# Kernel optimization log

Hardware: AMD Instinct MI355X
Metric: run time of the kernel (lower is better)

The kernel has to match this reference:

```python
import jax, jax.numpy as jnp
import numpy as np

B, S, IN, OUT = 4, 2048, 4096, 4096


def setup_inputs() -> dict:
    key = jax.random.key(0)
    k_x, k_q, k_s, k_z, k_b = jax.random.split(key, 5)
    x = jax.random.normal(k_x, (B, S, IN), dtype=jnp.float32)
    # packed int4 weights: each int holds two unsigned nibbles (inputs 2r and 2r+1)
    qweight = jax.random.randint(k_q, (IN // 2, OUT), 0, 256, dtype=jnp.int32)
    # per-output-channel scales (positive) and zeros (zeros = zero_point * scale in pack())
    scales = jax.random.uniform(k_s, (OUT, 1), minval=0.01, maxval=0.05, dtype=jnp.float32)
    zeros = jax.random.normal(k_z, (OUT, 1), dtype=jnp.float32) * 0.1
    bias = jax.random.normal(k_b, (OUT,), dtype=jnp.float32) * 0.02
    return {"x": x, "qweight": qweight, "scales": scales, "zeros": zeros, "bias": bias}


def _dequant_weight(qweight, scales, zeros):
    # unpack two 4-bit values per packed element along the input dim
    low = qweight & 0xF            # input index 2r
    high = (qweight >> 4) & 0xF    # input index 2r+1
    w_int = jnp.stack([low, high], axis=1).reshape(-1, qweight.shape[1])  # (IN, OUT)
    zp = jnp.round(zeros / scales)  # integer zero point per output channel, (OUT,1)
    # w = (q - zp) * scale, broadcast per output column
    return (w_int.astype(jnp.float32) - zp.T) * scales.T  # (IN, OUT)


def reference(x, qweight, scales, zeros, bias):
    w = _dequant_weight(qweight, scales, zeros)          # (IN, OUT) fp32
    y = jnp.einsum('bsi,io->bso', x.astype(jnp.float32), w) + bias
    return y.astype(x.dtype)
```

## Files before the change

### kernel.cpp

```cpp
#include <hip/hip_runtime.h>
#include <hip/hip_bf16.h>
#include <stdint.h>

#define M_TOT 8192
#define N_TOT 4096
#define K_TOT 4096
#define BM 128
#define BN 128
#define BKI 128
#define NTI (K_TOT / BKI)

typedef short s16x8 __attribute__((ext_vector_type(8)));
typedef float f32x4 __attribute__((ext_vector_type(4)));
typedef int   i32x4 __attribute__((ext_vector_type(4)));
typedef char  i8x16 __attribute__((ext_vector_type(16)));

__device__ __forceinline__ short f2bf(float f) {
    unsigned int u = __float_as_uint(f);
    u = (u + 0x7fffu + ((u >> 16) & 1u)) >> 16;
    return (short)u;
}

__device__ __forceinline__ void async_copy16(const void* g, void* l) {
    __builtin_amdgcn_global_load_lds(
        (const __attribute__((address_space(1))) void*)g,
        (__attribute__((address_space(3))) void*)l, 16, 0, 0);
}

__global__ __launch_bounds__(256)
void prep(const float* __restrict__ x, const int* __restrict__ qw,
          char* __restrict__ xq, char* __restrict__ wq,
          float* __restrict__ sxv, float* __restrict__ sumv) {
    __shared__ float rmax[4], rsum[4];
    __shared__ char tile[256 * 64];
    const int t = threadIdx.x;

    if (blockIdx.x < M_TOT) {
        const int row = blockIdx.x;
        const float* xp = x + (size_t)row * K_TOT + t * 16;
        f32x4 f[4];
        float amax = 0.f, sum = 0.f;
        #pragma unroll
        for (int i = 0; i < 4; ++i) {
            f[i] = *(const f32x4*)(xp + i * 4);
            #pragma unroll
            for (int j = 0; j < 4; ++j) {
                amax = fmaxf(amax, fabsf(f[i][j]));
                sum += f[i][j];
            }
        }
        #pragma unroll
        for (int s = 1; s < 64; s <<= 1) {
            amax = fmaxf(amax, __shfl_xor(amax, s, 64));
            sum += __shfl_xor(sum, s, 64);
        }
        const int wv = t >> 6;
        if ((t & 63) == 0) { rmax[wv] = amax; rsum[wv] = sum; }
        __syncthreads();
        amax = fmaxf(fmaxf(rmax[0], rmax[1]), fmaxf(rmax[2], rmax[3]));
        sum  = rsum[0] + rsum[1] + rsum[2] + rsum[3];
        const float inv = amax > 0.f ? 127.0f / amax : 0.f;
        i8x16 v;
        #pragma unroll
        for (int i = 0; i < 4; ++i)
            #pragma unroll
            for (int j = 0; j < 4; ++j)
                v[i * 4 + j] = (char)(int)rintf(f[i][j] * inv);
        *(i8x16*)&xq[(size_t)row * K_TOT + t * 16] = v;
        if (t == 0) { sxv[row] = amax * (1.0f / 127.0f); sumv[row] = sum; }
    } else {
        const int bq = blockIdx.x - M_TOT;
        const int o0 = (bq & 15) * 256;
        const int kb = bq >> 4;
        const int r0 = kb * 32;
        const int o  = o0 + t;
        #pragma unroll
        for (int g = 0; g < 4; ++g) {
            i8x16 v;
            #pragma unroll
            for (int p = 0; p < 8; ++p) {
                const int q = qw[(size_t)(r0 + g * 8 + p) * N_TOT + o];
                v[2 * p]     = (char)(q & 15);
                v[2 * p + 1] = (char)((q >> 4) & 15);
            }
            *(i8x16*)&tile[t * 64 + ((g ^ (t & 3)) << 4)] = v;
        }
        __syncthreads();
        #pragma unroll
        for (int it = 0; it < 4; ++it) {
            const int L = it * 256 + t;
            const int row = L >> 2, c = L & 3;
            *(i8x16*)&wq[(size_t)(o0 + row) * K_TOT + kb * 64 + c * 16] =
                *(const i8x16*)&tile[row * 64 + ((c ^ (row & 3)) << 4)];
        }
    }
}

__global__ __launch_bounds__(256, 2)
void gemm_i8(const char* __restrict__ xq, const char* __restrict__ wq,
             const float* __restrict__ sxv, const float* __restrict__ sumv,
             const float* __restrict__ scales, const float* __restrict__ zeros,
             const float* __restrict__ bias, float* __restrict__ out) {
    __shared__ __align__(16) char Sm8[32768];
    char* As = Sm8;
    char* Bs = Sm8 + 16384;

    const int tid = threadIdx.x;
    const int n0 = blockIdx.x * BN;
    const int m0 = blockIdx.y * BM;
    const int lane = tid & 63;
    const int wv = tid >> 6;
    const int wr = wv >> 1, wc = wv & 1;
    const int lrow = lane & 15, lk = lane >> 4;

    i32x4 acc[4][4] = {};

    for (int kt = 0; kt < NTI; ++kt) {
        const int k0 = kt * BKI;
        #pragma unroll
        for (int i = 0; i < 4; ++i) {
            const int g = i * 256 + wv * 64 + lane;
            const int row = g >> 3, c = g & 7;
            async_copy16(xq + (size_t)(m0 + row) * K_TOT + k0 + ((c ^ (row & 7)) << 4),
                         &As[(i * 256 + wv * 64) * 16]);
        }
        #pragma unroll
        for (int i = 0; i < 4; ++i) {
            const int g = i * 256 + wv * 64 + lane;
            const int row = g >> 3, c = g & 7;
            async_copy16(wq + (size_t)(n0 + row) * K_TOT + k0 + ((c ^ (row & 7)) << 4),
                         &Bs[(i * 256 + wv * 64) * 16]);
        }
        __syncthreads();

        #pragma unroll
        for (int ks = 0; ks < 2; ++ks) {
            const int slot = ks * 4 + lk;
            i32x4 a[4], b[4];
            #pragma unroll
            for (int mi = 0; mi < 4; ++mi) {
                const int row = wr * 64 + mi * 16 + lrow;
                a[mi] = *(const i32x4*)&As[row * 128 + ((slot ^ (row & 7)) << 4)];
            }
            #pragma unroll
            for (int ni = 0; ni < 4; ++ni) {
                const int row = wc * 64 + ni * 16 + lrow;
                b[ni] = *(const i32x4*)&Bs[row * 128 + ((slot ^ (row & 7)) << 4)];
            }
            #pragma unroll
            for (int mi = 0; mi < 4; ++mi)
                #pragma unroll
                for (int ni = 0; ni < 4; ++ni)
                    acc[mi][ni] = __builtin_amdgcn_mfma_i32_16x16x64_i8(
                        a[mi], b[ni], acc[mi][ni], 0, 0, 0);
        }
        __syncthreads();
    }

    float* fbuf = (float*)Sm8;
    float c0v[4], c1v[4], bsv[4];
    #pragma unroll
    for (int ni = 0; ni < 4; ++ni) {
        const int cg = n0 + wc * 64 + ni * 16 + lrow;
        const float c0 = scales[cg];
        c0v[ni] = c0;
        c1v[ni] = -rintf(zeros[cg] / c0) * c0;
        bsv[ni] = bias[cg];
    }
    #pragma unroll
    for (int p = 0; p < 2; ++p) {
        __syncthreads();
        #pragma unroll
        for (int q = 0; q < 2; ++q) {
            const int mi = 2 * p + q;
            const int rl = wr * 32 + q * 16 + lk * 4;
            #pragma unroll
            for (int j = 0; j < 4; ++j) {
                const int r = rl + j;
                const int gr = m0 + wr * 64 + mi * 16 + lk * 4 + j;
                const float sx = sxv[gr];
                const float Sx = sumv[gr];
                #pragma unroll
                for (int ni = 0; ni < 4; ++ni) {
                    const int col = wc * 64 + ni * 16 + lrow;
                    const float y = fmaf(c0v[ni] * sx, (float)acc[mi][ni][j],
                                         fmaf(c1v[ni], Sx, bsv[ni]));
                    fbuf[r * 128 + (col ^ (((r >> 2) & 1) << 4))] = y;
                }
            }
        }
        __syncthreads();
        #pragma unroll
        for (int rd = 0; rd < 8; ++rd) {
            const int L = rd * 256 + tid;
            const int r = L >> 5;
            const int c4 = (L & 31) * 4;
            const float4 v = *(const float4*)&fbuf[r * 128 + (c4 ^ (((r >> 2) & 1) << 4))];
            const int grow = m0 + (r >> 5) * 64 + p * 32 + (r & 31);
            *(float4*)&out[(size_t)grow * N_TOT + n0 + c4] = v;
        }
    }
}

__global__ __launch_bounds__(256, 2)
void qlin_fused(const float* __restrict__ x,
                const int* __restrict__ qw,
                const float* __restrict__ scales,
                const float* __restrict__ zeros,
                const float* __restrict__ bias,
                float* __restrict__ out) {
    __shared__ short As[128 * 64];
    __shared__ short Bs[128 * 64];

    const int tid = threadIdx.x;
    const int n0 = blockIdx.x * 128;
    const int m0 = blockIdx.y * 128;

    const int a_kg   = tid & 7;
    const int a_row0 = tid >> 3;
    const int b_oloc = tid & 127;
    const int b_rg0  = tid >> 7;

    const int ocol = n0 + b_oloc;
    const float c0 = scales[ocol];
    const float c1 = -rintf(zeros[ocol] / c0) * c0;

    const int lane = tid & 63;
    const int wv   = tid >> 6;
    const int wr   = wv >> 1;
    const int wc   = wv & 1;
    const int lrow = lane & 15;
    const int lk   = lane >> 4;

    f32x4 acc[4][4] = {};

    for (int kt = 0; kt < K_TOT / 64; ++kt) {
        const int k0 = kt * 64;
        {
            const float* srcb = x + (size_t)(m0)*K_TOT + k0 + a_kg * 8;
            #pragma unroll
            for (int i = 0; i < 4; ++i) {
                const int row = a_row0 + 32 * i;
                const float4 f0 = *(const float4*)(srcb + (size_t)row * K_TOT);
                const float4 f1 = *(const float4*)(srcb + (size_t)row * K_TOT + 4);
                s16x8 v;
                v[0] = f2bf(f0.x); v[1] = f2bf(f0.y); v[2] = f2bf(f0.z); v[3] = f2bf(f0.w);
                v[4] = f2bf(f1.x); v[5] = f2bf(f1.y); v[6] = f2bf(f1.z); v[7] = f2bf(f1.w);
                *(s16x8*)&As[row * 64 + ((a_kg ^ (row & 7)) << 3)] = v;
            }
        }
        {
            const int rbase = k0 >> 1;
            #pragma unroll
            for (int i = 0; i < 4; ++i) {
                const int rg = b_rg0 + 2 * i;
                const int* qp = qw + (size_t)(rbase + rg * 4) * N_TOT + ocol;
                s16x8 v;
                #pragma unroll
                for (int rr = 0; rr < 4; ++rr) {
                    const int q = qp[(size_t)rr * N_TOT];
                    v[2 * rr]     = f2bf(fmaf((float)(q & 15), c0, c1));
                    v[2 * rr + 1] = f2bf(fmaf((float)((q >> 4) & 15), c0, c1));
                }
                *(s16x8*)&Bs[b_oloc * 64 + ((rg ^ (b_oloc & 7)) << 3)] = v;
            }
        }
        __syncthreads();
        #pragma unroll
        for (int ks = 0; ks < 2; ++ks) {
            const int slot = ks * 4 + lk;
            s16x8 a[4], b[4];
            #pragma unroll
            for (int mi = 0; mi < 4; ++mi) {
                const int row = wr * 64 + mi * 16 + lrow;
                a[mi] = *(const s16x8*)&As[row * 64 + ((slot ^ (row & 7)) << 3)];
            }
            #pragma unroll
            for (int ni = 0; ni < 4; ++ni) {
                const int row = wc * 64 + ni * 16 + lrow;
                b[ni] = *(const s16x8*)&Bs[row * 64 + ((slot ^ (row & 7)) << 3)];
            }
            #pragma unroll
            for (int mi = 0; mi < 4; ++mi)
                #pragma unroll
                for (int ni = 0; ni < 4; ++ni)
                    acc[mi][ni] = __builtin_amdgcn_mfma_f32_16x16x32_bf16(
                        a[mi], b[ni], acc[mi][ni], 0, 0, 0);
        }
        __syncthreads();
    }

    #pragma unroll
    for (int mi = 0; mi < 4; ++mi) {
        const int rg = m0 + wr * 64 + mi * 16 + lk * 4;
        #pragma unroll
        for (int ni = 0; ni < 4; ++ni) {
            const int cg = n0 + wc * 64 + ni * 16 + lrow;
            const float bs = bias[cg];
            #pragma unroll
            for (int j = 0; j < 4; ++j)
                out[(size_t)(rg + j) * N_TOT + cg] = acc[mi][ni][j] + bs;
        }
    }
}

extern "C" void kernel_launch(void* const* d_in, const int* in_sizes, int n_in,
                              void* d_out, int out_size, void* d_ws, size_t ws_size,
                              hipStream_t stream) {
    const float* x      = (const float*)d_in[0];
    const int*   qw     = (const int*)d_in[1];
    const float* scales = (const float*)d_in[2];
    const float* zeros  = (const float*)d_in[3];
    const float* bias   = (const float*)d_in[4];
    float* out = (float*)d_out;

    const size_t XQ_BYTES = (size_t)M_TOT * K_TOT;
    const size_t WQ_BYTES = (size_t)N_TOT * K_TOT;
    const size_t SX_BYTES = (size_t)M_TOT * 4;
    const size_t NEED = XQ_BYTES + WQ_BYTES + 2 * SX_BYTES;

    if (ws_size >= NEED) {
        char*  xq   = (char*)d_ws;
        char*  wqt  = (char*)d_ws + XQ_BYTES;
        float* sxv  = (float*)((char*)d_ws + XQ_BYTES + WQ_BYTES);
        float* sumv = sxv + M_TOT;

        hipLaunchKernelGGL(prep, dim3(M_TOT + 1024), dim3(256), 0, stream,
                           x, qw, xq, wqt, sxv, sumv);
        hipLaunchKernelGGL(gemm_i8, dim3(N_TOT / BN, M_TOT / BM), dim3(256), 0, stream,
                           xq, wqt, sxv, sumv, scales, zeros, bias, out);
    } else {
        hipLaunchKernelGGL(qlin_fused, dim3(N_TOT / 128, M_TOT / 128), dim3(256), 0, stream,
                           x, qw, scales, zeros, bias, out);
    }
}
```

Baseline: 173.7 us.

## Double-buffer int8 GEMM with packed nibble weights, larger tiles and block swizzle

Reworks the int8 GEMM path in several ways. It keeps the weights packed as 4-bit nibbles in the workspace and unpacks them in registers, halving B-tile traffic, and permutes the activation quantization order to match. It moves to 256x128 tiles with 512 threads, double-buffers the LDS loads so the next tile loads while the current one computes, and adds s_setprio around the MFMAs and a block-index swizzle for L2 locality. The cost is more LDS per block (80 KB), extra ALU work for the nibble unpack, and higher register pressure under the new launch bounds.

```diff
diff --git a/kernel.cpp b/kernel.cpp
--- a/kernel.cpp
+++ b/kernel.cpp
@@ -5,15 +5,17 @@
 #define M_TOT 8192
 #define N_TOT 4096
 #define K_TOT 4096
-#define BM 128
+#define KP    (K_TOT / 2)
+#define BM 256
 #define BN 128
-#define BKI 128
-#define NTI (K_TOT / BKI)
+#define BK 128
+#define NTI (K_TOT / BK)
 
 typedef short s16x8 __attribute__((ext_vector_type(8)));
 typedef float f32x4 __attribute__((ext_vector_type(4)));
 typedef int   i32x4 __attribute__((ext_vector_type(4)));
 typedef char  i8x16 __attribute__((ext_vector_type(16)));
+typedef unsigned int u32;
 
 __device__ __forceinline__ short f2bf(float f) {
     unsigned int u = __float_as_uint(f);
@@ -29,13 +31,12 @@
 
 __global__ __launch_bounds__(256)
 void prep(const float* __restrict__ x, const int* __restrict__ qw,
-          char* __restrict__ xq, char* __restrict__ wq,
+          char* __restrict__ xq, unsigned char* __restrict__ wqp,
           float* __restrict__ sxv, float* __restrict__ sumv) {
-    __shared__ float rmax[4], rsum[4];
-    __shared__ char tile[256 * 64];
     const int t = threadIdx.x;
 
     if (blockIdx.x < M_TOT) {
+        __shared__ float rmax[4], rsum[4];
         const int row = blockIdx.x;
         const float* xp = x + (size_t)row * K_TOT + t * 16;
         f32x4 f[4];
@@ -62,102 +63,137 @@
         const float inv = amax > 0.f ? 127.0f / amax : 0.f;
         i8x16 v;
         #pragma unroll
-        for (int i = 0; i < 4; ++i)
-            #pragma unroll
-            for (int j = 0; j < 4; ++j)
-                v[i * 4 + j] = (char)(int)rintf(f[i][j] * inv);
+        for (int g = 0; g < 2; ++g)
+            #pragma unroll
+            for (int j = 0; j < 4; ++j) {
+                const int ke = g * 8 + 2 * j;
+                const int ko = ke + 1;
+                v[g * 8 + j]     = (char)(int)rintf(f[ke >> 2][ke & 3] * inv);
+                v[g * 8 + 4 + j] = (char)(int)rintf(f[ko >> 2][ko & 3] * inv);
+            }
         *(i8x16*)&xq[(size_t)row * K_TOT + t * 16] = v;
         if (t == 0) { sxv[row] = amax * (1.0f / 127.0f); sumv[row] = sum; }
     } else {
-        const int bq = blockIdx.x - M_TOT;
-        const int o0 = (bq & 15) * 256;
-        const int kb = bq >> 4;
-        const int r0 = kb * 32;
+        __shared__ int wtile[256][17];
+        const int wb = blockIdx.x - M_TOT;
+        const int o0 = (wb & 15) * 256;
+        const int r0 = (wb >> 4) * 64;
         const int o  = o0 + t;
         #pragma unroll
-        for (int g = 0; g < 4; ++g) {
-            i8x16 v;
-            #pragma unroll
-            for (int p = 0; p < 8; ++p) {
-                const int q = qw[(size_t)(r0 + g * 8 + p) * N_TOT + o];
-                v[2 * p]     = (char)(q & 15);
-                v[2 * p + 1] = (char)((q >> 4) & 15);
-            }
-            *(i8x16*)&tile[t * 64 + ((g ^ (t & 3)) << 4)] = v;
+        for (int c = 0; c < 16; ++c) {
+            u32 d = 0;
+            #pragma unroll
+            for (int b = 0; b < 4; ++b) {
+                const u32 q = (u32)qw[(size_t)(r0 + c * 4 + b) * N_TOT + o];
+                d |= (q & 255u) << (8 * b);
+            }
+            wtile[t][c] = (int)d;
         }
         __syncthreads();
         #pragma unroll
         for (int it = 0; it < 4; ++it) {
             const int L = it * 256 + t;
             const int row = L >> 2, c = L & 3;
-            *(i8x16*)&wq[(size_t)(o0 + row) * K_TOT + kb * 64 + c * 16] =
-                *(const i8x16*)&tile[row * 64 + ((c ^ (row & 3)) << 4)];
-        }
-    }
-}
-
-__global__ __launch_bounds__(256, 2)
-void gemm_i8(const char* __restrict__ xq, const char* __restrict__ wq,
+            const int4 vv = make_int4(wtile[row][c * 4], wtile[row][c * 4 + 1],
+                                      wtile[row][c * 4 + 2], wtile[row][c * 4 + 3]);
+            *(int4*)&wqp[(size_t)(o0 + row) * KP + r0 + c * 16] = vv;
+        }
+    }
+}
+
+__global__ __launch_bounds__(512, 4)
+void gemm_i8(const char* __restrict__ xq, const unsigned char* __restrict__ wqp,
              const float* __restrict__ sxv, const float* __restrict__ sumv,
              const float* __restrict__ scales, const float* __restrict__ zeros,
              const float* __restrict__ bias, float* __restrict__ out) {
-    __shared__ __align__(16) char Sm8[32768];
-    char* As = Sm8;
-    char* Bs = Sm8 + 16384;
+    __shared__ __align__(16) char Sm[81920];
+    char* const A0 = Sm;
+    char* const A1 = Sm + 32768;
+    char* const B0 = Sm + 65536;
+    char* const B1 = Sm + 73728;
 
     const int tid = threadIdx.x;
-    const int n0 = blockIdx.x * BN;
-    const int m0 = blockIdx.y * BM;
+    const int bid = blockIdx.x;
+    const int sw  = (bid & 7) * 128 + (bid >> 3);
+    const int n0  = (sw >> 5) * BN;
+    const int m0  = (sw & 31) * BM;
     const int lane = tid & 63;
-    const int wv = tid >> 6;
-    const int wr = wv >> 1, wc = wv & 1;
+    const int wid  = tid >> 6;
+    const int wr   = wid >> 1;
+    const int wc   = wid & 1;
     const int lrow = lane & 15, lk = lane >> 4;
 
     i32x4 acc[4][4] = {};
 
-    for (int kt = 0; kt < NTI; ++kt) {
-        const int k0 = kt * BKI;
+    auto stageA = [&](char* dst, int kt) {
+        const int k0 = kt * BK;
         #pragma unroll
         for (int i = 0; i < 4; ++i) {
-            const int g = i * 256 + wv * 64 + lane;
+            const int g = i * 512 + tid;
             const int row = g >> 3, c = g & 7;
             async_copy16(xq + (size_t)(m0 + row) * K_TOT + k0 + ((c ^ (row & 7)) << 4),
-                         &As[(i * 256 + wv * 64) * 16]);
-        }
-        #pragma unroll
-        for (int i = 0; i < 4; ++i) {
-            const int g = i * 256 + wv * 64 + lane;
-            const int row = g >> 3, c = g & 7;
-            async_copy16(wq + (size_t)(n0 + row) * K_TOT + k0 + ((c ^ (row & 7)) << 4),
-                         &Bs[(i * 256 + wv * 64) * 16]);
-        }
-        __syncthreads();
-
+                         dst + (i * 512 + wid * 64) * 16);
+        }
+    };
+    auto stageB = [&](char* dst, int kt) {
+        const int kp0 = kt * (BK / 2);
+        const int row = tid >> 2, G = tid & 3;
+        async_copy16(wqp + (size_t)(n0 + row) * KP + kp0 + ((G ^ (row & 3)) << 4),
+                     dst + (wid * 64) * 16);
+    };
+
+    auto compute = [&](const char* Ard, const char* Brd) {
         #pragma unroll
         for (int ks = 0; ks < 2; ++ks) {
             const int slot = ks * 4 + lk;
-            i32x4 a[4], b[4];
+            i32x4 a[4];
             #pragma unroll
             for (int mi = 0; mi < 4; ++mi) {
                 const int row = wr * 64 + mi * 16 + lrow;
-                a[mi] = *(const i32x4*)&As[row * 128 + ((slot ^ (row & 7)) << 4)];
-            }
+                a[mi] = *(const i32x4*)&Ard[row * 128 + ((slot ^ (row & 7)) << 4)];
+            }
+            i32x4 b[4];
             #pragma unroll
             for (int ni = 0; ni < 4; ++ni) {
                 const int row = wc * 64 + ni * 16 + lrow;
-                b[ni] = *(const i32x4*)&Bs[row * 128 + ((slot ^ (row & 7)) << 4)];
-            }
+                const int G = slot >> 1, sub = slot & 1;
+                const int off = row * 64 + ((G ^ (row & 3)) << 4) + (sub << 3);
+                const u32 d0 = *(const u32*)&Brd[off];
+                const u32 d1 = *(const u32*)&Brd[off + 4];
+                const u32 M = 0x0F0F0F0Fu;
+                b[ni][0] = (int)(d0 & M);
+                b[ni][1] = (int)((d0 >> 4) & M);
+                b[ni][2] = (int)(d1 & M);
+                b[ni][3] = (int)((d1 >> 4) & M);
+            }
+            __builtin_amdgcn_s_setprio(1);
             #pragma unroll
             for (int mi = 0; mi < 4; ++mi)
                 #pragma unroll
                 for (int ni = 0; ni < 4; ++ni)
                     acc[mi][ni] = __builtin_amdgcn_mfma_i32_16x16x64_i8(
                         a[mi], b[ni], acc[mi][ni], 0, 0, 0);
-        }
-        __syncthreads();
-    }
-
-    float* fbuf = (float*)Sm8;
+            __builtin_amdgcn_s_setprio(0);
+        }
+    };
+
+    stageA(A0, 0); stageB(B0, 0);
+    asm volatile("s_waitcnt vmcnt(0)" ::: "memory");
+    __builtin_amdgcn_s_barrier();
+
+    #pragma unroll 1
+    for (int t = 0; t < NTI; t += 2) {
+        if (t + 1 < NTI) { stageA(A1, t + 1); stageB(B1, t + 1); }
+        compute(A0, B0);
+        asm volatile("s_waitcnt vmcnt(0)" ::: "memory");
+        __builtin_amdgcn_s_barrier();
+        if (t + 2 < NTI) { stageA(A0, t + 2); stageB(B0, t + 2); }
+        compute(A1, B1);
+        asm volatile("s_waitcnt vmcnt(0)" ::: "memory");
+        __builtin_amdgcn_s_barrier();
+    }
+
+    float* fbuf = (float*)Sm;
     float c0v[4], c1v[4], bsv[4];
     #pragma unroll
     for (int ni = 0; ni < 4; ++ni) {
@@ -170,34 +206,33 @@
     #pragma unroll
     for (int p = 0; p < 2; ++p) {
         __syncthreads();
-        #pragma unroll
-        for (int q = 0; q < 2; ++q) {
-            const int mi = 2 * p + q;
-            const int rl = wr * 32 + q * 16 + lk * 4;
-            #pragma unroll
-            for (int j = 0; j < 4; ++j) {
-                const int r = rl + j;
-                const int gr = m0 + wr * 64 + mi * 16 + lk * 4 + j;
-                const float sx = sxv[gr];
-                const float Sx = sumv[gr];
+        if ((wr >> 1) == p) {
+            #pragma unroll
+            for (int mi = 0; mi < 4; ++mi) {
                 #pragma unroll
-                for (int ni = 0; ni < 4; ++ni) {
-                    const int col = wc * 64 + ni * 16 + lrow;
-                    const float y = fmaf(c0v[ni] * sx, (float)acc[mi][ni][j],
-                                         fmaf(c1v[ni], Sx, bsv[ni]));
-                    fbuf[r * 128 + (col ^ (((r >> 2) & 1) << 4))] = y;
+                for (int j = 0; j < 4; ++j) {
+                    const int rl = (wr & 1) * 64 + mi * 16 + lk * 4 + j;
+                    const int gr = m0 + p * 128 + rl;
+                    const float sx = sxv[gr];
+                    const float Sx = sumv[gr];
+                    #pragma unroll
+                    for (int ni = 0; ni < 4; ++ni) {
+                        const int col = wc * 64 + ni * 16 + lrow;
+                        const float y = fmaf(c0v[ni] * sx, (float)acc[mi][ni][j],
+                                             fmaf(c1v[ni], Sx, bsv[ni]));
+                        fbuf[rl * 128 + (col ^ (((rl >> 2) & 1) << 4))] = y;
+                    }
                 }
             }
         }
         __syncthreads();
         #pragma unroll
         for (int rd = 0; rd < 8; ++rd) {
-            const int L = rd * 256 + tid;
+            const int L = rd * 512 + tid;
             const int r = L >> 5;
             const int c4 = (L & 31) * 4;
             const float4 v = *(const float4*)&fbuf[r * 128 + (c4 ^ (((r >> 2) & 1) << 4))];
-            const int grow = m0 + (r >> 5) * 64 + p * 32 + (r & 31);
-            *(float4*)&out[(size_t)grow * N_TOT + n0 + c4] = v;
+            *(float4*)&out[(size_t)(m0 + p * 128 + r) * N_TOT + n0 + c4] = v;
         }
     }
 }
@@ -315,20 +350,20 @@
     float* out = (float*)d_out;
 
     const size_t XQ_BYTES = (size_t)M_TOT * K_TOT;
-    const size_t WQ_BYTES = (size_t)N_TOT * K_TOT;
+    const size_t WQ_BYTES = (size_t)N_TOT * KP;
     const size_t SX_BYTES = (size_t)M_TOT * 4;
     const size_t NEED = XQ_BYTES + WQ_BYTES + 2 * SX_BYTES;
 
     if (ws_size >= NEED) {
         char*  xq   = (char*)d_ws;
-        char*  wqt  = (char*)d_ws + XQ_BYTES;
+        unsigned char* wqp = (unsigned char*)d_ws + XQ_BYTES;
         float* sxv  = (float*)((char*)d_ws + XQ_BYTES + WQ_BYTES);
         float* sumv = sxv + M_TOT;
 
-        hipLaunchKernelGGL(prep, dim3(M_TOT + 1024), dim3(256), 0, stream,
-                           x, qw, xq, wqt, sxv, sumv);
-        hipLaunchKernelGGL(gemm_i8, dim3(N_TOT / BN, M_TOT / BM), dim3(256), 0, stream,
-                           xq, wqt, sxv, sumv, scales, zeros, bias, out);
+        hipLaunchKernelGGL(prep, dim3(M_TOT + 512), dim3(256), 0, stream,
+                           x, qw, xq, wqp, sxv, sumv);
+        hipLaunchKernelGGL(gemm_i8, dim3((M_TOT / BM) * (N_TOT / BN)), dim3(512), 0, stream,
+                           xq, wqp, sxv, sumv, scales, zeros, bias, out);
     } else {
         hipLaunchKernelGGL(qlin_fused, dim3(N_TOT / 128, M_TOT / 128), dim3(256), 0, stream,
                            x, qw, scales, zeros, bias, out);
```

Measured after the change: 316.9 us. 82.4% more time.
